# Performance work log

Hardware: AMD Instinct MI355X
Metric: run time of the kernel (lower is better)

The kernel has to match this reference:

```python
import jax, jax.numpy as jnp
import numpy as np

N_EMBD = 1024
N_HEAD = 16


def setup_inputs() -> dict:
    key = jax.random.key(0)
    ks = jax.random.split(key, 5)
    C = N_EMBD
    x = jax.random.normal(ks[0], (4, 2048, C), dtype=jnp.float32)
    # linear params, scaled like torch default init (~U(-1/sqrt(C),1/sqrt(C)))
    s = 1.0 / np.sqrt(C)
    W_attn = jax.random.uniform(ks[1], (C, 3 * C), jnp.float32, -s, s)
    b_attn = jax.random.uniform(ks[2], (3 * C,), jnp.float32, -s, s)
    W_proj = jax.random.uniform(ks[3], (C, C), jnp.float32, -s, s)
    b_proj = jax.random.uniform(ks[4], (C,), jnp.float32, -s, s)
    return {"x": x, "W_attn": W_attn, "b_attn": b_attn, "W_proj": W_proj, "b_proj": b_proj}


def reference(x, W_attn, b_attn, W_proj, b_proj):
    B, T, C = x.shape
    H = N_HEAD
    D = C // H
    qkv = x @ W_attn + b_attn                      # [B,T,3C]
    q, k, v = jnp.split(qkv, 3, axis=-1)
    # [B,T,C] -> [B,H,T,D]
    q = q.reshape(B, T, H, D).transpose(0, 2, 1, 3)
    k = k.reshape(B, T, H, D).transpose(0, 2, 1, 3)
    v = v.reshape(B, T, H, D).transpose(0, 2, 1, 3)
    scale = 1.0 / np.sqrt(D).astype(np.float32)
    att = jnp.einsum('bhqd,bhkd->bhqk', q, k) * scale  # [B,H,T,T]
    causal = jnp.tril(jnp.ones((T, T), dtype=bool))
    att = jnp.where(causal[None, None], att, -jnp.inf)
    att = jax.nn.softmax(att, axis=-1)
    y = jnp.einsum('bhqk,bhkd->bhqd', att, v)      # [B,H,T,D]
    y = y.transpose(0, 2, 1, 3).reshape(B, T, C)
    return y @ W_proj + b_proj
```

## Files before the change

kernel.cpp:

```cpp
#include <hip/hip_runtime.h>
#include <hip/hip_bf16.h>
#include <math.h>


typedef __bf16 bf16x8 __attribute__((ext_vector_type(8)));
typedef float f32x4 __attribute__((ext_vector_type(4)));
typedef float f32x16 __attribute__((ext_vector_type(16)));

__device__ __forceinline__ f32x4 mfma16(bf16x8 a, bf16x8 b, f32x4 c) {
    return __builtin_amdgcn_mfma_f32_16x16x32_bf16(a, b, c, 0, 0, 0);
}
__device__ __forceinline__ f32x16 mfma32(bf16x8 a, bf16x8 b, f32x16 c) {
    return __builtin_amdgcn_mfma_f32_32x32x16_bf16(a, b, c, 0, 0, 0);
}

#define GLOBAL_AS __attribute__((address_space(1)))
#define LDS_AS __attribute__((address_space(3)))

__device__ __forceinline__ void async_copy16(const __hip_bfloat16* g, __hip_bfloat16* l) {
    __builtin_amdgcn_global_load_lds((const GLOBAL_AS uint32_t*)g, (LDS_AS uint32_t*)l, 16, 0, 0);
}

__device__ __forceinline__ uint32_t cvtpk(float lo, float hi) {
    uint32_t r;
    asm("v_cvt_pk_bf16_f32 %0, %1, %2" : "=v"(r) : "v"(lo), "v"(hi));
    return r;
}

#define QSCL 0.18033688011112042f

__global__ __launch_bounds__(256) void cast_x_kernel(const float* __restrict__ in,
                                                     __hip_bfloat16* __restrict__ out, int n) {
    int i = (blockIdx.x * 256 + threadIdx.x) * 8;
    if (i >= n) return;
    union { __hip_bfloat16 h[8]; uint4 v; } tmp;
#pragma unroll
    for (int j = 0; j < 8; ++j) tmp.h[j] = __float2bfloat16(in[i + j]);
    *reinterpret_cast<uint4*>(out + i) = tmp.v;
}

__global__ __launch_bounds__(256) void transpose_cast_kernel(const float* __restrict__ in,
                                                             __hip_bfloat16* __restrict__ out,
                                                             int R, int Cc) {
    __shared__ float tile[32][33];
    int c0 = blockIdx.x * 32, r0 = blockIdx.y * 32;
    int tx = threadIdx.x & 31, ty = threadIdx.x >> 5;
#pragma unroll
    for (int i = 0; i < 4; ++i) {
        int r = r0 + ty + i * 8;
        tile[ty + i * 8][tx] = in[(size_t)r * Cc + c0 + tx];
    }
    __syncthreads();
#pragma unroll
    for (int i = 0; i < 4; ++i) {
        int c = c0 + ty + i * 8;
        out[(size_t)c * R + r0 + tx] = __float2bfloat16(tile[tx][ty + i * 8]);
    }
}

#define GEMM128_BODY(A_, Bt_, K_)                                                      \
    __shared__ __hip_bfloat16 As[2][128 * 32];                                         \
    __shared__ __hip_bfloat16 Bs[2][128 * 32];                                         \
    const int tid = threadIdx.x;                                                       \
    const int w = tid >> 6;                                                            \
    const int lr = tid & 15, lh = (tid & 63) >> 4;                                     \
    const int wr = w >> 1, wc = w & 1;                                                 \
    f32x4 zero = {0.f, 0.f, 0.f, 0.f};                                                 \
    f32x4 acc[4][4];                                                                   \
    _Pragma("unroll") for (int i = 0; i < 4; ++i)                                      \
        _Pragma("unroll") for (int j = 0; j < 4; ++j) acc[i][j] = zero;                \
    const int nt = (K_) >> 5;                                                          \
    auto stage_ = [&](int d_, int t_) {                                                \
        int kb = t_ * 32;                                                              \
        _Pragma("unroll") for (int ld = 0; ld < 2; ++ld) {                             \
            int s = ld * 256 + tid;                                                    \
            int row = s >> 2, ke = (s & 3) * 8;                                        \
            async_copy16((A_) + (size_t)(m0 + row) * (K_) + kb + ke,                   \
                         &As[d_][(ld * 256 + w * 64) * 8]);                            \
            async_copy16((Bt_) + (size_t)(n0 + row) * (K_) + kb + ke,                  \
                         &Bs[d_][(ld * 256 + w * 64) * 8]);                            \
        }                                                                              \
    };                                                                                 \
    stage_(0, 0);                                                                      \
    stage_(1, 1);                                                                      \
    asm volatile("s_waitcnt vmcnt(4)" ::: "memory");                                   \
    __builtin_amdgcn_s_barrier();                                                      \
    __builtin_amdgcn_sched_barrier(0);                                                 \
    for (int t = 0; t < nt; ++t) {                                                     \
        const int d = t & 1;                                                           \
        bf16x8 af[4], bf[4];                                                           \
        _Pragma("unroll") for (int mf = 0; mf < 4; ++mf)                               \
            af[mf] = *reinterpret_cast<const bf16x8*>(                                 \
                &As[d][(wr * 64 + mf * 16 + lr) * 32 + lh * 8]);                       \
        _Pragma("unroll") for (int nf = 0; nf < 4; ++nf)                               \
            bf[nf] = *reinterpret_cast<const bf16x8*>(                                 \
                &Bs[d][(wc * 64 + nf * 16 + lr) * 32 + lh * 8]);                       \
        _Pragma("unroll") for (int mf = 0; mf < 4; ++mf)                               \
            _Pragma("unroll") for (int nf = 0; nf < 4; ++nf)                           \
                acc[mf][nf] = mfma16(af[mf], bf[nf], acc[mf][nf]);                     \
        if (t + 1 < nt) __syncthreads();                                               \
        if (t + 2 < nt) stage_(d, t + 2);                                              \
    }

__global__ __launch_bounds__(256) void gemm_qkv_kernel(
    const __hip_bfloat16* __restrict__ A, const __hip_bfloat16* __restrict__ Bt,
    const float* __restrict__ bias,
    __hip_bfloat16* __restrict__ qd, __hip_bfloat16* __restrict__ kd,
    __hip_bfloat16* __restrict__ vtd) {
    const int K = 1024;
    const int m0 = blockIdx.x * 128;
    const int n0 = blockIdx.y * 128;
    GEMM128_BODY(A, Bt, K)

    const int region = n0 >> 10;
#pragma unroll
    for (int mf = 0; mf < 4; ++mf) {
#pragma unroll
        for (int nf = 0; nf < 4; ++nf) {
            int n = n0 + wc * 64 + nf * 16 + lr;
            float bv = bias[n];
            int mbase = m0 + wr * 64 + mf * 16 + 4 * lh;
            int bb = mbase >> 11;
            int t = mbase & 2047;
            int c = n & 1023, hh = c >> 6, dd = c & 63;
            if (region == 2) {
                union { __hip_bfloat16 h[4]; uint2 v; } pk;
#pragma unroll
                for (int r = 0; r < 4; ++r) pk.h[r] = __float2bfloat16(acc[mf][nf][r] + bv);
                *reinterpret_cast<uint2*>(
                    &vtd[(((size_t)bb * 16 + hh) * 64 + dd) * 2048 + t]) = pk.v;
            } else if (region == 0) {
#pragma unroll
                for (int r = 0; r < 4; ++r)
                    qd[(((size_t)bb * 16 + hh) * 2048 + t + r) * 64 + dd] =
                        __float2bfloat16((acc[mf][nf][r] + bv) * QSCL);
            } else {
#pragma unroll
                for (int r = 0; r < 4; ++r)
                    kd[(((size_t)bb * 16 + hh) * 2048 + t + r) * 64 + dd] =
                        __float2bfloat16(acc[mf][nf][r] + bv);
            }
        }
    }
}

__global__ __launch_bounds__(256) void gemm_proj_kernel(
    const __hip_bfloat16* __restrict__ A, const __hip_bfloat16* __restrict__ Bt,
    const float* __restrict__ bias, float* __restrict__ out) {
    const int K = 1024, N = 1024;
    const int m0 = blockIdx.x * 128;
    const int n0 = blockIdx.y * 128;
    GEMM128_BODY(A, Bt, K)

#pragma unroll
    for (int nf = 0; nf < 4; ++nf) {
        int n = n0 + wc * 64 + nf * 16 + lr;
        float bv = bias[n];
#pragma unroll
        for (int mf = 0; mf < 4; ++mf) {
            int mbase = m0 + wr * 64 + mf * 16 + 4 * lh;
#pragma unroll
            for (int r = 0; r < 4; ++r)
                out[(size_t)(mbase + r) * N + n] = acc[mf][nf][r] + bv;
        }
    }
}

__global__ __launch_bounds__(512) void attn_kernel(
    const __hip_bfloat16* __restrict__ q, const __hip_bfloat16* __restrict__ k,
    const __hip_bfloat16* __restrict__ vt, __hip_bfloat16* __restrict__ y) {
    const int T = 2048, D = 64, C = 1024;
    const float THR = 8.0f;

    int wid = ((int)blockIdx.x & 7) * 64 + ((int)blockIdx.x >> 3);
    int bh = wid >> 3;
    int qr = wid & 7;
    int q256 = (wid & 32) ? qr : 7 - qr;
    int b = bh >> 4, h = bh & 15;
    int tid = threadIdx.x;
    int w = tid >> 6, l = tid & 63;
    int ql = l & 31, hi = l >> 5;

    __shared__ __hip_bfloat16 Ks[64 * 64];
    __shared__ __hip_bfloat16 Vs[64 * 64];
    __shared__ __hip_bfloat16 Pt[8][32][36];

    const int q0 = q256 * 256 + w * 32;
    const __hip_bfloat16* kbh = k + (size_t)bh * T * D;
    const __hip_bfloat16* vbh = vt + (size_t)bh * D * T;

    bf16x8 qf[4];
#pragma unroll
    for (int c = 0; c < 4; ++c)
        qf[c] = *reinterpret_cast<const bf16x8*>(
            q + ((size_t)bh * T + q0 + ql) * D + c * 16 + hi * 8);

    f32x16 o0 = {}, o1 = {};
    float m = -INFINITY, lp = 0.f;

    const int lastSub = q0 >> 5;
    const int nt64 = 4 * q256 + 4;

    for (int t64 = 0; t64 < nt64; ++t64) {
        __syncthreads();
        {
            int slot = tid;
            int row = slot >> 3;
            int fold = ((row & 7) ^ (row >> 3)) & 7;
            int colb = ((slot & 7) * 16) ^ (fold << 4);
            async_copy16(kbh + (size_t)(t64 * 64 + row) * 64 + (colb >> 1),
                         Ks + (size_t)(w * 64) * 8);
            async_copy16(vbh + (size_t)row * T + t64 * 64 + (colb >> 1),
                         Vs + (size_t)(w * 64) * 8);
        }
        __syncthreads();

#pragma unroll
        for (int sub = 0; sub < 2; ++sub) {
            const int is = t64 * 2 + sub;
            if (is > lastSub) break;
            bf16x8 kf[4];
            {
                int krow = sub * 32 + ql;
                int kfold = ((krow & 7) ^ (krow >> 3)) & 7;
                const char* KsB = reinterpret_cast<const char*>(Ks) + krow * 128;
#pragma unroll
                for (int c = 0; c < 4; ++c)
                    kf[c] = *reinterpret_cast<const bf16x8*>(
                        KsB + ((c * 32 + hi * 16) ^ (kfold << 4)));
            }

            __builtin_amdgcn_s_setprio(1);
            f32x16 s = {};
            s = mfma32(kf[0], qf[0], s);
            s = mfma32(kf[1], qf[1], s);
            s = mfma32(kf[2], qf[2], s);
            s = mfma32(kf[3], qf[3], s);
            __builtin_amdgcn_s_setprio(0);

            bf16x8 vf[2][2];
#pragma unroll
            for (int dblk = 0; dblk < 2; ++dblk) {
                int vrow = dblk * 32 + ql;
                int vfold = ((vrow & 7) ^ (vrow >> 3)) & 7;
                const char* VsB = reinterpret_cast<const char*>(Vs) + vrow * 128;
#pragma unroll
                for (int sl = 0; sl < 2; ++sl)
                    vf[dblk][sl] = *reinterpret_cast<const bf16x8*>(
                        VsB + ((sub * 64 + sl * 32 + hi * 16) ^ (vfold << 4)));
            }

            if (is == lastSub) {
#pragma unroll
                for (int r = 0; r < 16; ++r) {
                    int kvrow = (r & 3) + 8 * (r >> 2) + 4 * hi;
                    if (kvrow > ql) s[r] = -INFINITY;
                }
            }

            float mx;
            {
                float a = fmaxf(fmaxf(s[0], s[1]), s[2]);
                float bq = fmaxf(fmaxf(s[3], s[4]), s[5]);
                float c = fmaxf(fmaxf(s[6], s[7]), s[8]);
                float d = fmaxf(fmaxf(s[9], s[10]), s[11]);
                float e = fmaxf(fmaxf(s[12], s[13]), s[14]);
                mx = fmaxf(fmaxf(fmaxf(a, bq), fmaxf(c, d)), fmaxf(e, s[15]));
            }
            mx = fmaxf(mx, __shfl_xor(mx, 32));

            if (!__all(mx - m <= THR)) {
                float mnew = fmaxf(m, mx);
                float al = __builtin_amdgcn_exp2f(m - mnew);
                m = mnew;
                lp *= al;
#pragma unroll
                for (int r = 0; r < 16; ++r) { o0[r] *= al; o1[r] *= al; }
            }

#pragma unroll
            for (int r = 0; r < 16; ++r) s[r] = __builtin_amdgcn_exp2f(s[r] - m);

            lp += ((s[0] + s[1]) + (s[2] + s[3])) + ((s[4] + s[5]) + (s[6] + s[7])) +
                  (((s[8] + s[9]) + (s[10] + s[11])) + ((s[12] + s[13]) + (s[14] + s[15])));

            {
                uint2 w0, w1, w2, w3;
                w0.x = cvtpk(s[0], s[1]);   w0.y = cvtpk(s[2], s[3]);
                w1.x = cvtpk(s[4], s[5]);   w1.y = cvtpk(s[6], s[7]);
                w2.x = cvtpk(s[8], s[9]);   w2.y = cvtpk(s[10], s[11]);
                w3.x = cvtpk(s[12], s[13]); w3.y = cvtpk(s[14], s[15]);
                *reinterpret_cast<uint2*>(&Pt[w][ql][4 * hi])      = w0;
                *reinterpret_cast<uint2*>(&Pt[w][ql][8 + 4 * hi])  = w1;
                *reinterpret_cast<uint2*>(&Pt[w][ql][16 + 4 * hi]) = w2;
                *reinterpret_cast<uint2*>(&Pt[w][ql][24 + 4 * hi]) = w3;
            }

            union { uint32_t u[4]; bf16x8 v; } pa0, pa1;
            {
                uint2 r0 = *reinterpret_cast<const uint2*>(&Pt[w][ql][8 * hi]);
                uint2 r1 = *reinterpret_cast<const uint2*>(&Pt[w][ql][8 * hi + 4]);
                uint2 r2 = *reinterpret_cast<const uint2*>(&Pt[w][ql][16 + 8 * hi]);
                uint2 r3 = *reinterpret_cast<const uint2*>(&Pt[w][ql][16 + 8 * hi + 4]);
                pa0.u[0] = r0.x; pa0.u[1] = r0.y; pa0.u[2] = r1.x; pa0.u[3] = r1.y;
                pa1.u[0] = r2.x; pa1.u[1] = r2.y; pa1.u[2] = r3.x; pa1.u[3] = r3.y;
            }

            __builtin_amdgcn_s_setprio(1);
            o0 = mfma32(vf[0][0], pa0.v, o0);
            o0 = mfma32(vf[0][1], pa1.v, o0);
            o1 = mfma32(vf[1][0], pa0.v, o1);
            o1 = mfma32(vf[1][1], pa1.v, o1);
            __builtin_amdgcn_s_setprio(0);
        }
    }

    lp += __shfl_xor(lp, 32);
    float inv = 1.0f / lp;

    __hip_bfloat16* yq = y + ((size_t)b * T + q0 + ql) * C + h * 64;
#pragma unroll
    for (int dblk = 0; dblk < 2; ++dblk) {
#pragma unroll
        for (int g = 0; g < 4; ++g) {
            union { __hip_bfloat16 h4[4]; uint2 v; } pkk;
#pragma unroll
            for (int r = 0; r < 4; ++r) {
                float val = (dblk ? o1[g * 4 + r] : o0[g * 4 + r]) * inv;
                pkk.h4[r] = __float2bfloat16(val);
            }
            *reinterpret_cast<uint2*>(yq + dblk * 32 + g * 8 + hi * 4) = pkk.v;
        }
    }
}

extern "C" void kernel_launch(void* const* d_in, const int* in_sizes, int n_in,
                              void* d_out, int out_size, void* d_ws, size_t ws_size,
                              hipStream_t stream) {
    const float* x      = (const float*)d_in[0];
    const float* W_attn = (const float*)d_in[1];
    const float* b_attn = (const float*)d_in[2];
    const float* W_proj = (const float*)d_in[3];
    const float* b_proj = (const float*)d_in[4];
    float* out = (float*)d_out;

    __hip_bfloat16* wsb = reinterpret_cast<__hip_bfloat16*>(d_ws);
    __hip_bfloat16* xb  = wsb;
    __hip_bfloat16* WaT = xb + (size_t)8192 * 1024;
    __hip_bfloat16* WpT = WaT + (size_t)3072 * 1024;
    __hip_bfloat16* qd  = WpT + (size_t)1024 * 1024;
    __hip_bfloat16* kd  = qd + (size_t)64 * 2048 * 64;
    __hip_bfloat16* vtd = kd + (size_t)64 * 2048 * 64;
    __hip_bfloat16* ya  = vtd + (size_t)64 * 2048 * 64;

    cast_x_kernel<<<4096, 256, 0, stream>>>(x, xb, 8192 * 1024);
    transpose_cast_kernel<<<dim3(96, 32), 256, 0, stream>>>(W_attn, WaT, 1024, 3072);
    transpose_cast_kernel<<<dim3(32, 32), 256, 0, stream>>>(W_proj, WpT, 1024, 1024);
    gemm_qkv_kernel<<<dim3(64, 24), 256, 0, stream>>>(xb, WaT, b_attn, qd, kd, vtd);
    attn_kernel<<<512, 512, 0, stream>>>(qd, kd, vtd, ya);
    gemm_proj_kernel<<<dim3(64, 8), 256, 0, stream>>>(ya, WpT, b_proj, out);
}
```

Before: 171.3 us.

## Rewrite QKV GEMM with 256x256 tiles, swizzled LDS and interleaved prefetch

Replaces the 128x128 QKV projection GEMM with a 256x256 tile per 512-thread block using K-step 64. Operands are staged through an XOR-swizzled double-buffered LDS layout, and next-tile async copies are interleaved with MFMA phases under fine-grained vmcnt waits and setprio. This raises operand reuse per block and overlaps global loads with compute. The cost is 128 KB of LDS, more accumulator registers, and a 384-block grid that may fill the CUs unevenly.

```diff
diff --git a/kernel.cpp b/kernel.cpp
--- a/kernel.cpp
+++ b/kernel.cpp
@@ -102,42 +102,109 @@
         if (t + 2 < nt) stage_(d, t + 2);                                              \
     }
 
-__global__ __launch_bounds__(256) void gemm_qkv_kernel(
+__global__ __launch_bounds__(512, 2) void gemm_qkv_kernel(
     const __hip_bfloat16* __restrict__ A, const __hip_bfloat16* __restrict__ Bt,
     const float* __restrict__ bias,
     __hip_bfloat16* __restrict__ qd, __hip_bfloat16* __restrict__ kd,
     __hip_bfloat16* __restrict__ vtd) {
-    const int K = 1024;
-    const int m0 = blockIdx.x * 128;
-    const int n0 = blockIdx.y * 128;
-    GEMM128_BODY(A, Bt, K)
+    const int K = 1024, nt = 16;
+    const int m0 = blockIdx.x * 256;
+    const int n0 = blockIdx.y * 256;
+    const int tid = threadIdx.x;
+    const int w = tid >> 6, l = tid & 63;
+    const int lr = l & 15, lh = l >> 4;
+    const int wr = w >> 2, wcn = w & 3;
+
+    __shared__ __hip_bfloat16 S[2][8][64 * 64];
+
+    f32x4 acc[8][4] = {};
+
+    auto stageQ = [&](int d, int qi, int t) {
+        const __hip_bfloat16* src = (qi < 4)
+            ? A + (size_t)(m0 + qi * 64) * K
+            : Bt + (size_t)(n0 + (qi - 4) * 64) * K;
+        int row = tid >> 3;
+        int colb = ((tid & 7) * 16) ^ ((row & 7) << 4);
+        async_copy16(src + (size_t)row * K + t * 64 + (colb >> 1),
+                     &S[d][qi][(w * 64) * 8]);
+    };
+
+    stageQ(0, 4, 0); stageQ(0, 5, 0); stageQ(0, 6, 0); stageQ(0, 7, 0);
+    stageQ(0, 0, 0); stageQ(0, 2, 0); stageQ(0, 1, 0); stageQ(0, 3, 0);
+    asm volatile("s_waitcnt vmcnt(2)" ::: "memory");
+    __builtin_amdgcn_s_barrier();
+
+    const int aq = wr * 2;
+    const int bq = 4 + wcn;
+
+    for (int t = 0; t < nt; ++t) {
+        const int d = t & 1, e = d ^ 1;
+        const bool nxt = (t + 1 < nt);
+#pragma unroll
+        for (int p = 0; p < 4; ++p) {
+            const int mh = p >> 1, kk = p & 1;
+            bf16x8 af[4], bf[4];
+            const __hip_bfloat16* Ab = &S[d][aq + mh][0];
+            const __hip_bfloat16* Bb = &S[d][bq][0];
+            const int colb = (kk * 64 + lh * 16) ^ ((lr & 7) << 4);
+#pragma unroll
+            for (int j = 0; j < 4; ++j) {
+                af[j] = *reinterpret_cast<const bf16x8*>(Ab + (j * 16 + lr) * 64 + (colb >> 1));
+                bf[j] = *reinterpret_cast<const bf16x8*>(Bb + (j * 16 + lr) * 64 + (colb >> 1));
+            }
+            if (nxt) {
+                const int pf0[4] = {4, 6, 0, 1};
+                const int pf1[4] = {5, 7, 2, 3};
+                stageQ(e, pf0[p], t + 1);
+                stageQ(e, pf1[p], t + 1);
+            }
+            __builtin_amdgcn_s_barrier();
+            asm volatile("s_waitcnt lgkmcnt(0)" ::: "memory");
+            __builtin_amdgcn_sched_barrier(0);
+            __builtin_amdgcn_s_setprio(1);
+#pragma unroll
+            for (int j = 0; j < 4; ++j)
+#pragma unroll
+                for (int nf = 0; nf < 4; ++nf)
+                    acc[mh * 4 + j][nf] = mfma16(af[j], bf[nf], acc[mh * 4 + j][nf]);
+            __builtin_amdgcn_s_setprio(0);
+            if (p == 1) {
+                if (nxt) asm volatile("s_waitcnt vmcnt(4)" ::: "memory");
+                else     asm volatile("s_waitcnt vmcnt(0)" ::: "memory");
+            } else if (p == 3) {
+                if (nxt) asm volatile("s_waitcnt vmcnt(2)" ::: "memory");
+                else     asm volatile("s_waitcnt vmcnt(0)" ::: "memory");
+            }
+            __builtin_amdgcn_s_barrier();
+        }
+    }
 
     const int region = n0 >> 10;
 #pragma unroll
-    for (int mf = 0; mf < 4; ++mf) {
+    for (int mf = 0; mf < 8; ++mf) {
 #pragma unroll
         for (int nf = 0; nf < 4; ++nf) {
-            int n = n0 + wc * 64 + nf * 16 + lr;
+            int n = n0 + wcn * 64 + nf * 16 + lr;
             float bv = bias[n];
-            int mbase = m0 + wr * 64 + mf * 16 + 4 * lh;
+            int mbase = m0 + wr * 128 + mf * 16 + 4 * lh;
             int bb = mbase >> 11;
-            int t = mbase & 2047;
+            int tt = mbase & 2047;
             int c = n & 1023, hh = c >> 6, dd = c & 63;
             if (region == 2) {
                 union { __hip_bfloat16 h[4]; uint2 v; } pk;
 #pragma unroll
                 for (int r = 0; r < 4; ++r) pk.h[r] = __float2bfloat16(acc[mf][nf][r] + bv);
                 *reinterpret_cast<uint2*>(
-                    &vtd[(((size_t)bb * 16 + hh) * 64 + dd) * 2048 + t]) = pk.v;
+                    &vtd[(((size_t)bb * 16 + hh) * 64 + dd) * 2048 + tt]) = pk.v;
             } else if (region == 0) {
 #pragma unroll
                 for (int r = 0; r < 4; ++r)
-                    qd[(((size_t)bb * 16 + hh) * 2048 + t + r) * 64 + dd] =
+                    qd[(((size_t)bb * 16 + hh) * 2048 + tt + r) * 64 + dd] =
                         __float2bfloat16((acc[mf][nf][r] + bv) * QSCL);
             } else {
 #pragma unroll
                 for (int r = 0; r < 4; ++r)
-                    kd[(((size_t)bb * 16 + hh) * 2048 + t + r) * 64 + dd] =
+                    kd[(((size_t)bb * 16 + hh) * 2048 + tt + r) * 64 + dd] =
                         __float2bfloat16(acc[mf][nf][r] + bv);
             }
         }
@@ -356,7 +423,7 @@
     cast_x_kernel<<<4096, 256, 0, stream>>>(x, xb, 8192 * 1024);
     transpose_cast_kernel<<<dim3(96, 32), 256, 0, stream>>>(W_attn, WaT, 1024, 3072);
     transpose_cast_kernel<<<dim3(32, 32), 256, 0, stream>>>(W_proj, WpT, 1024, 1024);
-    gemm_qkv_kernel<<<dim3(64, 24), 256, 0, stream>>>(xb, WaT, b_attn, qd, kd, vtd);
+    gemm_qkv_kernel<<<dim3(32, 12), 512, 0, stream>>>(xb, WaT, b_attn, qd, kd, vtd);
     attn_kernel<<<512, 512, 0, stream>>>(qd, kd, vtd, ya);
     gemm_proj_kernel<<<dim3(64, 8), 256, 0, stream>>>(ya, WpT, b_proj, out);
 }
```

Result: no change. 174.2 us (+1.7%).
